# Kernel tuning notes

Hardware: AMD Instinct MI355X
Metric: run time of the kernel (lower is better)

Reference implementation:

```python
import jax, jax.numpy as jnp
import numpy as np

B, C, S, F = 128, 5, 512, 3
U = 256          # encoder units
RU = 2 * U       # decoder units / bidirectional encoder width


def _lstm_cell(x_t, h, c, Wk, Wr, b):
    # Keras LSTM gate order: i, f, g(cell), o
    z = x_t @ Wk + h @ Wr + b
    i, f, g, o = jnp.split(z, 4, axis=-1)
    c_new = jax.nn.sigmoid(f) * c + jax.nn.sigmoid(i) * jnp.tanh(g)
    h_new = jax.nn.sigmoid(o) * jnp.tanh(c_new)
    return h_new, c_new


def _masked_lstm(xs, mask, Wk, Wr, b, units):
    # xs: [B,S,D], mask: [B,S] bool. Keras semantics: masked steps carry
    # previous state and previous output (== previous h for LSTM).
    Bn = xs.shape[0]

    def step(carry, inp):
        h, c = carry
        x_t, m_t = inp
        h_n, c_n = _lstm_cell(x_t, h, c, Wk, Wr, b)
        m = m_t[:, None]
        h2 = jnp.where(m, h_n, h)
        c2 = jnp.where(m, c_n, c)
        return (h2, c2), h2

    init = (jnp.zeros((Bn, units), xs.dtype), jnp.zeros((Bn, units), xs.dtype))
    _, outs = jax.lax.scan(step, init, (jnp.swapaxes(xs, 0, 1), mask.T))
    return jnp.swapaxes(outs, 0, 1)  # [B,S,units]


def setup_inputs() -> dict:
    key = jax.random.key(0)
    k = jax.random.split(key, 10)
    s = 0.05
    rn = lambda kk, sh: jax.random.normal(kk, sh, jnp.float32) * s
    return {
        "x": jax.random.normal(k[0], (B, C, S, F), jnp.float32),
        "Wf_k": rn(k[1], (C, 4 * U)), "Wf_r": rn(k[2], (U, 4 * U)), "bf": jnp.zeros((4 * U,), jnp.float32),
        "Wb_k": rn(k[3], (C, 4 * U)), "Wb_r": rn(k[4], (U, 4 * U)), "bb": jnp.zeros((4 * U,), jnp.float32),
        "Wd_k": rn(k[5], (C, 4 * RU)), "Wd_r": rn(k[6], (RU, 4 * RU)), "bd": jnp.zeros((4 * RU,), jnp.float32),
        "W_attn": rn(k[7], (RU + C, 1)), "b_attn": jnp.zeros((1,), jnp.float32),
        "W_dense": rn(k[8], (RU + RU, C)), "b_dense": jnp.zeros((C,), jnp.float32),
    }


def reference(x, Wf_k, Wf_r, bf, Wb_k, Wb_r, bb, Wd_k, Wd_r, bd,
              W_attn, b_attn, W_dense, b_dense):
    xt = jnp.transpose(x, (0, 2, 1, 3))          # [B,S,C,F]
    mask = xt[:, :, 0, 2] != 0                   # tf.cast(..., bool)
    xs = xt[:, :, :, 0]                          # [B,S,C]

    fwd = _masked_lstm(xs, mask, Wf_k, Wf_r, bf, U)
    bwd = _masked_lstm(xs[:, ::-1], mask[:, ::-1], Wb_k, Wb_r, bb, U)[:, ::-1]
    enc = jnp.concatenate([fwd, bwd], axis=-1)   # [B,S,RU]

    # attention(concat([tile(x_t), enc])) is linear -> split the weight:
    Wx, We = W_attn[:C, 0], W_attn[C:, 0]
    enc_scores = jnp.einsum('bsd,d->bs', enc, We) + b_attn[0]  # [B,S]

    hidden0 = enc[:, -1, :]                      # [B,RU]
    x0 = xs[:, 0, :]                             # [B,C]

    def dec_step(carry, _):
        hidden, x_t = carry
        scores = enc_scores + (x_t @ Wx)[:, None]             # [B,S]
        alpha = jax.nn.softmax(scores, axis=1)
        attn = jnp.einsum('bs,bsd->bd', alpha, enc)           # [B,RU]
        # decoder LSTM on a single timestep, initial_state=[hidden, attn]
        h_new, _c = _lstm_cell(x_t, hidden, attn, Wd_k, Wd_r, bd)
        x_new = jnp.concatenate([h_new, attn], axis=-1) @ W_dense + b_dense
        return (h_new, x_new), x_new

    _, ys = jax.lax.scan(dec_step, (hidden0, x0), None, length=S - 1)  # [S-1,B,C]
    return jnp.transpose(ys, (1, 2, 0))[..., None]           # [B,C,S-1,1]
```

## Files before the change

### kernel.cpp

```cpp
#include <hip/hip_runtime.h>
#include <math.h>

#define BATCH 128
#define CCH 5
#define SEQ 512
#define UNITS 256
#define RU 512

#define ENC_N 33554432

__device__ __forceinline__ float sigmoidf_(float v) {
    return 1.0f / (1.0f + __expf(-v));
}
__device__ __forceinline__ float tanhf_(float v) {
    float e = __expf(2.0f * v);
    return 1.0f - 2.0f / (e + 1.0f);
}
__device__ __forceinline__ void astoref(float* p, float v) {
    __hip_atomic_store(p, v, __ATOMIC_RELAXED, __HIP_MEMORY_SCOPE_AGENT);
}
__device__ __forceinline__ void astorei(int* p, int v) {
    __hip_atomic_store(p, v, __ATOMIC_RELAXED, __HIP_MEMORY_SCOPE_AGENT);
}
__device__ __forceinline__ unsigned long long aloadu64(const unsigned long long* p) {
    return __hip_atomic_load(p, __ATOMIC_RELAXED, __HIP_MEMORY_SCOPE_AGENT);
}
__device__ __forceinline__ int aloadi(const int* p) {
    return __hip_atomic_load(p, __ATOMIC_RELAXED, __HIP_MEMORY_SCOPE_AGENT);
}

__global__ __attribute__((amdgpu_flat_work_group_size(1024, 1024),
                          amdgpu_waves_per_eu(4, 4)))
void encoder_kernel(const float* __restrict__ x,
                    const float* __restrict__ Wf_k, const float* __restrict__ Wf_r,
                    const float* __restrict__ bf,
                    const float* __restrict__ Wb_k, const float* __restrict__ Wb_r,
                    const float* __restrict__ bb,
                    float* __restrict__ enc, float* __restrict__ h_ex,
                    int* __restrict__ flags)
{
    const int bid  = blockIdx.x;
    const int dir  = bid >> 7;
    const int tile = (bid >> 3) & 15;
    const int jsl  = bid & 7;
    const int grp  = dir * 16 + tile;
    const int bg0  = tile * 8;
    const float* __restrict__ Wk   = dir ? Wb_k : Wf_k;
    const float* __restrict__ Wr   = dir ? Wb_r : Wf_r;
    const float* __restrict__ bias = dir ? bb : bf;
    const int tid  = threadIdx.x;
    const int wv   = tid >> 6;
    const int lane = tid & 63;
    const int g0 = ((lane >> 5) << 8) + jsl * 32 + (lane & 31);

    __shared__ float zp[16][8][128];
    __shared__ float __align__(16) hL[8][260];
    __shared__ float WkL[5][128];
    __shared__ float biasL[128];
    __shared__ unsigned char mL[8][SEQ];
    __shared__ float xLe[8][8];
    __shared__ float padE[512];

    for (int i = tid; i < 8 * 260; i += 1024) ((float*)hL)[i] = 0.0f;
    if (tid < 512) padE[tid] = 0.0f;
    if (tid < 128) biasL[tid] = bias[((tid >> 5) << 8) + jsl * 32 + (tid & 31)];
    if (tid >= 128 && tid < 768) {
        int i = tid - 128, c = i >> 7, cl = i & 127;
        WkL[c][cl] = Wk[c * 1024 + ((cl >> 5) << 8) + jsl * 32 + (cl & 31)];
    }
    for (int i = tid; i < 8 * SEQ; i += 1024) {
        int b = i >> 9, tt = i & (SEQ - 1);
        mL[b][tt] = (x[((size_t)((bg0 + b) * CCH) * SEQ + tt) * 3 + 2] != 0.0f) ? 1 : 0;
    }
    float wr0[16], wr1[16];
    {
        const float* wbase = Wr + (size_t)(wv * 16) * 1024 + g0;
        #pragma unroll
        for (int r = 0; r < 16; ++r) {
            wr0[r] = wbase[(size_t)r * 1024];
            wr1[r] = wbase[(size_t)r * 1024 + 512];
        }
        #pragma unroll
        for (int r = 0; r < 16; ++r)
            asm volatile("" : "+v"(wr0[r]), "+v"(wr1[r]));
    }
    float creg = 0.0f;
    __syncthreads();

    for (int t = 0; t < SEQ; ++t) {
        const int ts = dir ? (SEQ - 1 - t) : t;
        if (t > 0 && wv < 8) {
            const int* fp = &flags[(grp * 8 + wv) * 32];
            if (lane == 0) {
                int guard = 0;
                while (aloadi(fp) < t && guard < (1 << 26)) {
                    __builtin_amdgcn_s_sleep(1); ++guard;
                }
            }
            int b = lane >> 3, u = wv * 32 + (lane & 7) * 4;
            const unsigned long long* hsrc = (const unsigned long long*)
                &h_ex[(size_t)(dir * 2 + ((t - 1) & 1)) * (BATCH * UNITS)
                      + (size_t)(bg0 + b) * UNITS + u];
            unsigned long long v0 = aloadu64(hsrc);
            unsigned long long v1 = aloadu64(hsrc + 1);
            *(unsigned long long*)&hL[b][u]     = v0;
            *(unsigned long long*)&hL[b][u + 2] = v1;
        }
        if (tid >= 960 && tid < 1000) {
            int i = tid - 960, b = i / 5, c = i - b * 5;
            xLe[b][c] = x[((size_t)((bg0 + b) * CCH + c) * SEQ + ts) * 3];
        }
        __syncthreads();

        float accA[8], accB[8];
        #pragma unroll
        for (int b = 0; b < 8; ++b) {
            float a0 = 0.f, a1 = 0.f;
            const float4* hp = (const float4*)&hL[b][wv * 16];
            #pragma unroll
            for (int q = 0; q < 4; ++q) {
                float4 h4 = hp[q];
                a0 = fmaf(h4.x, wr0[4*q+0], a0); a1 = fmaf(h4.x, wr1[4*q+0], a1);
                a0 = fmaf(h4.y, wr0[4*q+1], a0); a1 = fmaf(h4.y, wr1[4*q+1], a1);
                a0 = fmaf(h4.z, wr0[4*q+2], a0); a1 = fmaf(h4.z, wr1[4*q+2], a1);
                a0 = fmaf(h4.w, wr0[4*q+3], a0); a1 = fmaf(h4.w, wr1[4*q+3], a1);
            }
            accA[b] = a0; accB[b] = a1;
        }
        #pragma unroll
        for (int b = 0; b < 8; ++b) {
            zp[wv][b][lane]      = accA[b];
            zp[wv][b][64 + lane] = accB[b];
        }
        __syncthreads();

        if (tid < 256) {
            int b = tid >> 5, u = tid & 31;
            float zi = biasL[u], zf = biasL[32 + u], zg = biasL[64 + u], zo = biasL[96 + u];
            #pragma unroll
            for (int s = 0; s < 16; ++s) {
                zi += zp[s][b][u];       zf += zp[s][b][32 + u];
                zg += zp[s][b][64 + u];  zo += zp[s][b][96 + u];
            }
            #pragma unroll
            for (int c = 0; c < 5; ++c) {
                float xv = xLe[b][c];
                zi = fmaf(xv, WkL[c][u], zi);      zf = fmaf(xv, WkL[c][32 + u], zf);
                zg = fmaf(xv, WkL[c][64 + u], zg); zo = fmaf(xv, WkL[c][96 + u], zo);
            }
            float cn = sigmoidf_(zf) * creg + sigmoidf_(zi) * tanhf_(zg);
            float hn = sigmoidf_(zo) * tanhf_(cn);
            float hprev = hL[b][jsl * 32 + u];
            float h2 = mL[b][ts] ? hn : hprev;
            float c2 = mL[b][ts] ? cn : creg;
            creg = c2;
            astoref(&h_ex[(size_t)(dir * 2 + (t & 1)) * (BATCH * UNITS)
                          + (size_t)(bg0 + b) * UNITS + jsl * 32 + u], h2);
            enc[((size_t)(bg0 + b) * SEQ + ts) * RU + dir * UNITS + jsl * 32 + u] = h2;
        }
        __syncthreads();
        if (tid == 0) astorei(&flags[(grp * 8 + jsl) * 32], t + 1);
    }
    if (aloadi(&flags[(grp * 8 + jsl) * 32]) == -1) enc[0] = padE[tid & 511];
}

__global__ __launch_bounds__(256)
void attn_kernel(const float* __restrict__ enc,
                 const float* __restrict__ W_attn, const float* __restrict__ b_attn,
                 const float* __restrict__ W_dense, const float* __restrict__ b_dense,
                 const float* __restrict__ x,
                 float* __restrict__ attn_ws, float* __restrict__ hidden_ws,
                 float* __restrict__ xbuf, float* __restrict__ xconst)
{
    const int b = blockIdx.x;
    const int tid = threadIdx.x;
    const int lane = tid & 63;
    const int wv = tid >> 6;

    __shared__ float WeL[RU];
    __shared__ float scoresL[SEQ];
    __shared__ float red[256];
    __shared__ float attnL[RU];

    WeL[tid]       = W_attn[CCH + tid];
    WeL[tid + 256] = W_attn[CCH + tid + 256];
    __syncthreads();

    const float* __restrict__ encb = enc + (size_t)b * SEQ * RU;
    const float batt = b_attn[0];

    for (int s = wv; s < SEQ; s += 4) {
        const float* row = encb + (size_t)s * RU;
        float p = 0.0f;
        #pragma unroll
        for (int i = 0; i < 8; ++i) {
            int d = lane * 8 + i;
            p = fmaf(row[d], WeL[d], p);
        }
        #pragma unroll
        for (int o = 32; o; o >>= 1) p += __shfl_xor(p, o);
        if (lane == 0) scoresL[s] = p + batt;
    }
    __syncthreads();

    float m = fmaxf(scoresL[tid], scoresL[tid + 256]);
    red[tid] = m;
    __syncthreads();
    for (int st = 128; st; st >>= 1) {
        if (tid < st) red[tid] = fmaxf(red[tid], red[tid + st]);
        __syncthreads();
    }
    const float mx = red[0];
    __syncthreads();
    float e0 = __expf(scoresL[tid] - mx);
    float e1 = __expf(scoresL[tid + 256] - mx);
    red[tid] = e0 + e1;
    __syncthreads();
    for (int st = 128; st; st >>= 1) {
        if (tid < st) red[tid] += red[tid + st];
        __syncthreads();
    }
    const float sinv = 1.0f / red[0];
    __syncthreads();
    scoresL[tid]       = e0 * sinv;
    scoresL[tid + 256] = e1 * sinv;
    __syncthreads();

    float a0 = 0.0f, a1 = 0.0f;
    for (int s = 0; s < SEQ; ++s) {
        float al = scoresL[s];
        a0 = fmaf(al, encb[(size_t)s * RU + tid], a0);
        a1 = fmaf(al, encb[(size_t)s * RU + tid + 256], a1);
    }
    attn_ws[(size_t)b * RU + tid]       = a0;
    attn_ws[(size_t)b * RU + tid + 256] = a1;
    attnL[tid] = a0;
    attnL[tid + 256] = a1;
    hidden_ws[(size_t)b * RU + tid]       = encb[(size_t)(SEQ - 1) * RU + tid];
    hidden_ws[(size_t)b * RU + tid + 256] = encb[(size_t)(SEQ - 1) * RU + tid + 256];
    if (tid < CCH) xbuf[b * CCH + tid] = x[((size_t)(b * CCH + tid) * SEQ + 0) * 3];
    __syncthreads();

    if (tid < CCH) {
        float acc = b_dense[tid];
        for (int d = 0; d < RU; ++d)
            acc = fmaf(attnL[d], W_dense[(RU + d) * CCH + tid], acc);
        xconst[b * CCH + tid] = acc;
    }
}

__global__ __attribute__((amdgpu_flat_work_group_size(1024, 1024),
                          amdgpu_waves_per_eu(4, 4)))
void decoder_kernel(const float* __restrict__ Wd_k, const float* __restrict__ Wd_r,
                    const float* __restrict__ bd,
                    const float* __restrict__ W_dense,
                    const float* __restrict__ attn_ws, const float* __restrict__ hidden_ws,
                    const float* __restrict__ xbuf, const float* __restrict__ xconst,
                    float* __restrict__ h_ex, int* __restrict__ flags,
                    float* __restrict__ out)
{
    const int bid  = blockIdx.x;
    const int tile = bid >> 4;
    const int jsl  = bid & 15;
    const int bg0  = tile * 8;
    const int tid  = threadIdx.x;
    const int wv   = tid >> 6;
    const int lane = tid & 63;
    const int g0 = ((lane >> 5) << 9) + jsl * 32 + (lane & 31);

    __shared__ float zp[16][8][128];
    __shared__ float __align__(16) hL[8][516];
    __shared__ float WdL[RU * CCH];
    __shared__ float WkL[5][128];
    __shared__ float biasL[128];
    __shared__ float attL[8][32];
    __shared__ float xL[8][8], xcL[8][8];

    for (int i = tid; i < RU * CCH; i += 1024) WdL[i] = W_dense[i];
    if (tid < 128) biasL[tid] = bd[((tid >> 5) << 9) + jsl * 32 + (tid & 31)];
    if (tid >= 128 && tid < 768) {
        int i = tid - 128, c = i >> 7, cl = i & 127;
        WkL[c][cl] = Wd_k[c * 2048 + ((cl >> 5) << 9) + jsl * 32 + (cl & 31)];
    }
    if (tid < 256) {
        int b = tid >> 5, u = tid & 31;
        attL[b][u] = attn_ws[(size_t)(bg0 + b) * RU + jsl * 32 + u];
    }
    if (tid < 64) {
        int b = tid >> 3, c = tid & 7;
        if (c < 5) {
            xL[b][c]  = xbuf[(bg0 + b) * CCH + c];
            xcL[b][c] = xconst[(bg0 + b) * CCH + c];
        }
    }
    {
        int f = tid * 4, b = f >> 9, u = f & (RU - 1);
        float4 v = *(const float4*)&hidden_ws[(size_t)(bg0 + b) * RU + u];
        *(float4*)&hL[b][u] = v;
    }
    float wr0[32], wr1[32];
    {
        const float* wbase = Wd_r + (size_t)(wv * 32) * 2048 + g0;
        #pragma unroll
        for (int r = 0; r < 32; ++r) {
            wr0[r] = wbase[(size_t)r * 2048];
            wr1[r] = wbase[(size_t)r * 2048 + 1024];
        }
        #pragma unroll
        for (int r = 0; r < 32; ++r)
            asm volatile("" : "+v"(wr0[r]), "+v"(wr1[r]));
    }
    __syncthreads();

    for (int t = 0; t < SEQ; ++t) {
        if (t > 0) {
            const int* fp = &flags[(tile * 16 + wv) * 32];
            if (lane == 0) {
                int guard = 0;
                while (aloadi(fp) < t && guard < (1 << 26)) {
                    __builtin_amdgcn_s_sleep(1); ++guard;
                }
            }
            int b = lane >> 3, u = wv * 32 + (lane & 7) * 4;
            const unsigned long long* hsrc = (const unsigned long long*)
                &h_ex[(size_t)((t - 1) & 1) * (BATCH * RU)
                      + (size_t)(bg0 + b) * RU + u];
            unsigned long long v0 = aloadu64(hsrc);
            unsigned long long v1 = aloadu64(hsrc + 1);
            *(unsigned long long*)&hL[b][u]     = v0;
            *(unsigned long long*)&hL[b][u + 2] = v1;
            __syncthreads();

            for (int it = wv; it < 40; it += 16) {
                int bb = it / 5, c = it - bb * 5;
                float p = 0.f;
                #pragma unroll
                for (int q = 0; q < 8; ++q) {
                    int uu = lane + (q << 6);
                    p = fmaf(hL[bb][uu], WdL[uu * CCH + c], p);
                }
                #pragma unroll
                for (int o = 32; o; o >>= 1) p += __shfl_xor(p, o);
                if (lane == 0) {
                    float xn = p + xcL[bb][c];
                    xL[bb][c] = xn;
                    if (jsl == 0)
                        out[(size_t)((bg0 + bb) * CCH + c) * (SEQ - 1) + (t - 1)] = xn;
                }
            }
            if (t == 511) break;
        }

        float accA[8], accB[8];
        #pragma unroll
        for (int b = 0; b < 8; ++b) {
            float a0 = 0.f, a1 = 0.f;
            const float4* hp = (const float4*)&hL[b][wv * 32];
            #pragma unroll
            for (int q = 0; q < 8; ++q) {
                float4 h4 = hp[q];
                a0 = fmaf(h4.x, wr0[4*q+0], a0); a1 = fmaf(h4.x, wr1[4*q+0], a1);
                a0 = fmaf(h4.y, wr0[4*q+1], a0); a1 = fmaf(h4.y, wr1[4*q+1], a1);
                a0 = fmaf(h4.z, wr0[4*q+2], a0); a1 = fmaf(h4.z, wr1[4*q+2], a1);
                a0 = fmaf(h4.w, wr0[4*q+3], a0); a1 = fmaf(h4.w, wr1[4*q+3], a1);
            }
            accA[b] = a0; accB[b] = a1;
        }
        #pragma unroll
        for (int b = 0; b < 8; ++b) {
            zp[wv][b][lane]      = accA[b];
            zp[wv][b][64 + lane] = accB[b];
        }
        __syncthreads();

        if (tid < 256) {
            int b = tid >> 5, u = tid & 31;
            float zi = biasL[u], zf = biasL[32 + u], zg = biasL[64 + u], zo = biasL[96 + u];
            #pragma unroll
            for (int s = 0; s < 16; ++s) {
                zi += zp[s][b][u];       zf += zp[s][b][32 + u];
                zg += zp[s][b][64 + u];  zo += zp[s][b][96 + u];
            }
            #pragma unroll
            for (int c = 0; c < 5; ++c) {
                float xv = xL[b][c];
                zi = fmaf(xv, WkL[c][u], zi);      zf = fmaf(xv, WkL[c][32 + u], zf);
                zg = fmaf(xv, WkL[c][64 + u], zg); zo = fmaf(xv, WkL[c][96 + u], zo);
            }
            float cn = sigmoidf_(zf) * attL[b][u] + sigmoidf_(zi) * tanhf_(zg);
            float hn = sigmoidf_(zo) * tanhf_(cn);
            astoref(&h_ex[(size_t)(t & 1) * (BATCH * RU)
                          + (size_t)(bg0 + b) * RU + jsl * 32 + u], hn);
        }
        __syncthreads();
        if (tid == 0) astorei(&flags[(tile * 16 + jsl) * 32], t + 1);
    }
}

extern "C" void kernel_launch(void* const* d_in, const int* in_sizes, int n_in,
                              void* d_out, int out_size, void* d_ws, size_t ws_size,
                              hipStream_t stream)
{
    const float* x       = (const float*)d_in[0];
    const float* Wf_k    = (const float*)d_in[1];
    const float* Wf_r    = (const float*)d_in[2];
    const float* bf      = (const float*)d_in[3];
    const float* Wb_k    = (const float*)d_in[4];
    const float* Wb_r    = (const float*)d_in[5];
    const float* bb      = (const float*)d_in[6];
    const float* Wd_k    = (const float*)d_in[7];
    const float* Wd_r    = (const float*)d_in[8];
    const float* bd      = (const float*)d_in[9];
    const float* W_attn  = (const float*)d_in[10];
    const float* b_attn  = (const float*)d_in[11];
    const float* W_dense = (const float*)d_in[12];
    const float* b_dense = (const float*)d_in[13];
    float* out = (float*)d_out;

    float* ws = (float*)d_ws;
    float* enc      = ws;
    float* attn_p   = ws + ENC_N;
    float* hidden_p = ws + ENC_N + 65536;
    float* xbuf_p   = ws + ENC_N + 131072;
    float* xconst_p = ws + ENC_N + 131712;
    float* h_ex_e   = ws + ENC_N;
    int*   flag_e   = (int*)(ws + ENC_N + 131072);
    int*   flag_d   = (int*)ws;
    float* h_ex_d   = ws + 8192;

    hipMemsetAsync(flag_e, 0, 8192 * sizeof(int), stream);
    encoder_kernel<<<256, 1024, 0, stream>>>(x, Wf_k, Wf_r, bf, Wb_k, Wb_r, bb,
                                             enc, h_ex_e, flag_e);
    attn_kernel<<<BATCH, 256, 0, stream>>>(enc, W_attn, b_attn, W_dense, b_dense, x,
                                           attn_p, hidden_p, xbuf_p, xconst_p);
    hipMemsetAsync(flag_d, 0, 8192 * sizeof(int), stream);
    decoder_kernel<<<256, 1024, 0, stream>>>(Wd_k, Wd_r, bd, W_dense,
                                             attn_p, hidden_p, xbuf_p, xconst_p,
                                             h_ex_d, flag_d, out);
}
```

Measured before the change: 5.270 ms.

## Double-buffer hidden state, parallelize gate reduction, replace trailing barrier with counter

Both the encoder and decoder recurrent kernels now double-buffer the shared hidden-state tile, which lets them drop the end-of-step __syncthreads. The finishing waves publish the inter-block flag through a workgroup-scope atomic counter after their global stores have drained. The 16-way partial-sum reduction is now spread across all 1024 threads into a zred buffer, replacing the 256 threads that each summed four gates. In the decoder, the dense output projection overlaps with the recurrent matvec and its store moves to other threads, and the final step is peeled out of the loop. The aim is to shorten the per-timestep critical path in the latency-bound recurrence, at the cost of an extra barrier, more shared memory, and a spin-wait ordering subtlety.

```diff
diff --git a/kernel.cpp b/kernel.cpp
--- a/kernel.cpp
+++ b/kernel.cpp
@@ -53,16 +53,17 @@
     const int lane = tid & 63;
     const int g0 = ((lane >> 5) << 8) + jsl * 32 + (lane & 31);
 
-    __shared__ float zp[16][8][128];
-    __shared__ float __align__(16) hL[8][260];
+    __shared__ float2 zpP[16][8][64];
+    __shared__ float __align__(16) hLe[2][8][260];
+    __shared__ float zred[8][128];
     __shared__ float WkL[5][128];
     __shared__ float biasL[128];
     __shared__ unsigned char mL[8][SEQ];
     __shared__ float xLe[8][8];
-    __shared__ float padE[512];
-
-    for (int i = tid; i < 8 * 260; i += 1024) ((float*)hL)[i] = 0.0f;
-    if (tid < 512) padE[tid] = 0.0f;
+    __shared__ int msync;
+
+    for (int i = tid; i < 2 * 8 * 260; i += 1024) ((float*)hLe)[i] = 0.0f;
+    if (tid == 0) msync = 0;
     if (tid < 128) biasL[tid] = bias[((tid >> 5) << 8) + jsl * 32 + (tid & 31)];
     if (tid >= 128 && tid < 768) {
         int i = tid - 128, c = i >> 7, cl = i & 127;
@@ -88,6 +89,7 @@
     __syncthreads();
 
     for (int t = 0; t < SEQ; ++t) {
+        const int cur = t & 1;
         const int ts = dir ? (SEQ - 1 - t) : t;
         if (t > 0 && wv < 8) {
             const int* fp = &flags[(grp * 8 + wv) * 32];
@@ -103,8 +105,8 @@
                       + (size_t)(bg0 + b) * UNITS + u];
             unsigned long long v0 = aloadu64(hsrc);
             unsigned long long v1 = aloadu64(hsrc + 1);
-            *(unsigned long long*)&hL[b][u]     = v0;
-            *(unsigned long long*)&hL[b][u + 2] = v1;
+            *(unsigned long long*)&hLe[cur][b][u]     = v0;
+            *(unsigned long long*)&hLe[cur][b][u + 2] = v1;
         }
         if (tid >= 960 && tid < 1000) {
             int i = tid - 960, b = i / 5, c = i - b * 5;
@@ -116,7 +118,7 @@
         #pragma unroll
         for (int b = 0; b < 8; ++b) {
             float a0 = 0.f, a1 = 0.f;
-            const float4* hp = (const float4*)&hL[b][wv * 16];
+            const float4* hp = (const float4*)&hLe[cur][b][wv * 16];
             #pragma unroll
             for (int q = 0; q < 4; ++q) {
                 float4 h4 = hp[q];
@@ -128,40 +130,54 @@
             accA[b] = a0; accB[b] = a1;
         }
         #pragma unroll
-        for (int b = 0; b < 8; ++b) {
-            zp[wv][b][lane]      = accA[b];
-            zp[wv][b][64 + lane] = accB[b];
+        for (int b = 0; b < 8; ++b)
+            zpP[wv][b][lane] = make_float2(accA[b], accB[b]);
+        __syncthreads();
+
+        {
+            int b = tid >> 7, cl = tid & 127;
+            int gate = cl >> 5, u = cl & 31;
+            int lane_r = ((gate & 1) << 5) | u;
+            int comp = gate >> 1;
+            const float* zf = (const float*)zpP + b * 128 + lane_r * 2 + comp;
+            float sum = biasL[cl];
+            #pragma unroll
+            for (int s = 0; s < 16; ++s) sum += zf[s * 1024];
+            #pragma unroll
+            for (int c = 0; c < 5; ++c) sum = fmaf(xLe[b][c], WkL[c][cl], sum);
+            zred[b][cl] = sum;
         }
         __syncthreads();
 
         if (tid < 256) {
             int b = tid >> 5, u = tid & 31;
-            float zi = biasL[u], zf = biasL[32 + u], zg = biasL[64 + u], zo = biasL[96 + u];
-            #pragma unroll
-            for (int s = 0; s < 16; ++s) {
-                zi += zp[s][b][u];       zf += zp[s][b][32 + u];
-                zg += zp[s][b][64 + u];  zo += zp[s][b][96 + u];
-            }
-            #pragma unroll
-            for (int c = 0; c < 5; ++c) {
-                float xv = xLe[b][c];
-                zi = fmaf(xv, WkL[c][u], zi);      zf = fmaf(xv, WkL[c][32 + u], zf);
-                zg = fmaf(xv, WkL[c][64 + u], zg); zo = fmaf(xv, WkL[c][96 + u], zo);
-            }
-            float cn = sigmoidf_(zf) * creg + sigmoidf_(zi) * tanhf_(zg);
+            float zi = zred[b][u];
+            float zf_ = zred[b][32 + u];
+            float zg = zred[b][64 + u];
+            float zo = zred[b][96 + u];
+            float cn = sigmoidf_(zf_) * creg + sigmoidf_(zi) * tanhf_(zg);
             float hn = sigmoidf_(zo) * tanhf_(cn);
-            float hprev = hL[b][jsl * 32 + u];
+            float hprev = hLe[cur][b][jsl * 32 + u];
             float h2 = mL[b][ts] ? hn : hprev;
             float c2 = mL[b][ts] ? cn : creg;
             creg = c2;
             astoref(&h_ex[(size_t)(dir * 2 + (t & 1)) * (BATCH * UNITS)
                           + (size_t)(bg0 + b) * UNITS + jsl * 32 + u], h2);
             enc[((size_t)(bg0 + b) * SEQ + ts) * RU + dir * UNITS + jsl * 32 + u] = h2;
-        }
-        __syncthreads();
-        if (tid == 0) astorei(&flags[(grp * 8 + jsl) * 32], t + 1);
-    }
-    if (aloadi(&flags[(grp * 8 + jsl) * 32]) == -1) enc[0] = padE[tid & 511];
+            if (lane == 0) {
+                asm volatile("s_waitcnt vmcnt(0)" ::: "memory");
+                __hip_atomic_fetch_add(&msync, 1, __ATOMIC_RELAXED,
+                                       __HIP_MEMORY_SCOPE_WORKGROUP);
+            }
+            if (tid == 0) {
+                int target = 4 * (t + 1), guard = 0;
+                while (__hip_atomic_load(&msync, __ATOMIC_RELAXED,
+                                         __HIP_MEMORY_SCOPE_WORKGROUP) < target &&
+                       guard < (1 << 26)) ++guard;
+                astorei(&flags[(grp * 8 + jsl) * 32], t + 1);
+            }
+        }
+    }
 }
 
 __global__ __launch_bounds__(256)
@@ -268,15 +284,18 @@
     const int lane = tid & 63;
     const int g0 = ((lane >> 5) << 9) + jsl * 32 + (lane & 31);
 
-    __shared__ float zp[16][8][128];
-    __shared__ float __align__(16) hL[8][516];
+    __shared__ float2 zpP[16][8][64];
+    __shared__ float __align__(16) hLd[2][8][516];
+    __shared__ float zred[8][128];
     __shared__ float WdL[RU * CCH];
     __shared__ float WkL[5][128];
     __shared__ float biasL[128];
     __shared__ float attL[8][32];
     __shared__ float xL[8][8], xcL[8][8];
+    __shared__ int msync;
 
     for (int i = tid; i < RU * CCH; i += 1024) WdL[i] = W_dense[i];
+    if (tid == 0) msync = 0;
     if (tid < 128) biasL[tid] = bd[((tid >> 5) << 9) + jsl * 32 + (tid & 31)];
     if (tid >= 128 && tid < 768) {
         int i = tid - 128, c = i >> 7, cl = i & 127;
@@ -296,7 +315,7 @@
     {
         int f = tid * 4, b = f >> 9, u = f & (RU - 1);
         float4 v = *(const float4*)&hidden_ws[(size_t)(bg0 + b) * RU + u];
-        *(float4*)&hL[b][u] = v;
+        *(float4*)&hLd[0][b][u] = v;
     }
     float wr0[32], wr1[32];
     {
@@ -312,7 +331,8 @@
     }
     __syncthreads();
 
-    for (int t = 0; t < SEQ; ++t) {
+    for (int t = 0; t < SEQ - 1; ++t) {
+        const int cur = t & 1;
         if (t > 0) {
             const int* fp = &flags[(tile * 16 + wv) * 32];
             if (lane == 0) {
@@ -327,35 +347,16 @@
                       + (size_t)(bg0 + b) * RU + u];
             unsigned long long v0 = aloadu64(hsrc);
             unsigned long long v1 = aloadu64(hsrc + 1);
-            *(unsigned long long*)&hL[b][u]     = v0;
-            *(unsigned long long*)&hL[b][u + 2] = v1;
-            __syncthreads();
-
-            for (int it = wv; it < 40; it += 16) {
-                int bb = it / 5, c = it - bb * 5;
-                float p = 0.f;
-                #pragma unroll
-                for (int q = 0; q < 8; ++q) {
-                    int uu = lane + (q << 6);
-                    p = fmaf(hL[bb][uu], WdL[uu * CCH + c], p);
-                }
-                #pragma unroll
-                for (int o = 32; o; o >>= 1) p += __shfl_xor(p, o);
-                if (lane == 0) {
-                    float xn = p + xcL[bb][c];
-                    xL[bb][c] = xn;
-                    if (jsl == 0)
-                        out[(size_t)((bg0 + bb) * CCH + c) * (SEQ - 1) + (t - 1)] = xn;
-                }
-            }
-            if (t == 511) break;
-        }
+            *(unsigned long long*)&hLd[cur][b][u]     = v0;
+            *(unsigned long long*)&hLd[cur][b][u + 2] = v1;
+        }
+        __syncthreads();
 
         float accA[8], accB[8];
         #pragma unroll
         for (int b = 0; b < 8; ++b) {
             float a0 = 0.f, a1 = 0.f;
-            const float4* hp = (const float4*)&hL[b][wv * 32];
+            const float4* hp = (const float4*)&hLd[cur][b][wv * 32];
             #pragma unroll
             for (int q = 0; q < 8; ++q) {
                 float4 h4 = hp[q];
@@ -367,33 +368,104 @@
             accA[b] = a0; accB[b] = a1;
         }
         #pragma unroll
-        for (int b = 0; b < 8; ++b) {
-            zp[wv][b][lane]      = accA[b];
-            zp[wv][b][64 + lane] = accB[b];
+        for (int b = 0; b < 8; ++b)
+            zpP[wv][b][lane] = make_float2(accA[b], accB[b]);
+
+        if (t > 0) {
+            for (int it = wv; it < 40; it += 16) {
+                int bb = it / 5, c = it - bb * 5;
+                float p = 0.f;
+                #pragma unroll
+                for (int q = 0; q < 8; ++q) {
+                    int uu = lane + (q << 6);
+                    p = fmaf(hLd[cur][bb][uu], WdL[uu * CCH + c], p);
+                }
+                #pragma unroll
+                for (int o = 32; o; o >>= 1) p += __shfl_xor(p, o);
+                if (lane == 0) xL[bb][c] = p + xcL[bb][c];
+            }
+        }
+        __syncthreads();
+
+        {
+            int b = tid >> 7, cl = tid & 127;
+            int gate = cl >> 5, u = cl & 31;
+            int lane_r = ((gate & 1) << 5) | u;
+            int comp = gate >> 1;
+            const float* zf = (const float*)zpP + b * 128 + lane_r * 2 + comp;
+            float sum = biasL[cl];
+            #pragma unroll
+            for (int s = 0; s < 16; ++s) sum += zf[s * 1024];
+            #pragma unroll
+            for (int c = 0; c < 5; ++c) sum = fmaf(xL[b][c], WkL[c][cl], sum);
+            zred[b][cl] = sum;
         }
         __syncthreads();
 
         if (tid < 256) {
             int b = tid >> 5, u = tid & 31;
-            float zi = biasL[u], zf = biasL[32 + u], zg = biasL[64 + u], zo = biasL[96 + u];
-            #pragma unroll
-            for (int s = 0; s < 16; ++s) {
-                zi += zp[s][b][u];       zf += zp[s][b][32 + u];
-                zg += zp[s][b][64 + u];  zo += zp[s][b][96 + u];
-            }
-            #pragma unroll
-            for (int c = 0; c < 5; ++c) {
-                float xv = xL[b][c];
-                zi = fmaf(xv, WkL[c][u], zi);      zf = fmaf(xv, WkL[c][32 + u], zf);
-                zg = fmaf(xv, WkL[c][64 + u], zg); zo = fmaf(xv, WkL[c][96 + u], zo);
-            }
-            float cn = sigmoidf_(zf) * attL[b][u] + sigmoidf_(zi) * tanhf_(zg);
+            float zi = zred[b][u];
+            float zf_ = zred[b][32 + u];
+            float zg = zred[b][64 + u];
+            float zo = zred[b][96 + u];
+            float cn = sigmoidf_(zf_) * attL[b][u] + sigmoidf_(zi) * tanhf_(zg);
             float hn = sigmoidf_(zo) * tanhf_(cn);
             astoref(&h_ex[(size_t)(t & 1) * (BATCH * RU)
                           + (size_t)(bg0 + b) * RU + jsl * 32 + u], hn);
-        }
-        __syncthreads();
-        if (tid == 0) astorei(&flags[(tile * 16 + jsl) * 32], t + 1);
+            if (lane == 0) {
+                asm volatile("s_waitcnt vmcnt(0)" ::: "memory");
+                __hip_atomic_fetch_add(&msync, 1, __ATOMIC_RELAXED,
+                                       __HIP_MEMORY_SCOPE_WORKGROUP);
+            }
+            if (tid == 0) {
+                int target = 4 * (t + 1), guard = 0;
+                while (__hip_atomic_load(&msync, __ATOMIC_RELAXED,
+                                         __HIP_MEMORY_SCOPE_WORKGROUP) < target &&
+                       guard < (1 << 26)) ++guard;
+                astorei(&flags[(tile * 16 + jsl) * 32], t + 1);
+            }
+        }
+        if (t > 0 && jsl == 0 && tid >= 256 && tid < 296) {
+            int i = tid - 256, bb = i / 5, c = i - bb * 5;
+            out[(size_t)((bg0 + bb) * CCH + c) * (SEQ - 1) + (t - 1)] = xL[bb][c];
+        }
+    }
+
+    {
+        const int t = SEQ - 1;
+        const int cur = t & 1;
+        const int* fp = &flags[(tile * 16 + wv) * 32];
+        if (lane == 0) {
+            int guard = 0;
+            while (aloadi(fp) < t && guard < (1 << 26)) {
+                __builtin_amdgcn_s_sleep(1); ++guard;
+            }
+        }
+        int b = lane >> 3, u = wv * 32 + (lane & 7) * 4;
+        const unsigned long long* hsrc = (const unsigned long long*)
+            &h_ex[(size_t)((t - 1) & 1) * (BATCH * RU)
+                  + (size_t)(bg0 + b) * RU + u];
+        unsigned long long v0 = aloadu64(hsrc);
+        unsigned long long v1 = aloadu64(hsrc + 1);
+        *(unsigned long long*)&hLd[cur][b][u]     = v0;
+        *(unsigned long long*)&hLd[cur][b][u + 2] = v1;
+        __syncthreads();
+        if (jsl == 0) {
+            for (int it = wv; it < 40; it += 16) {
+                int bb = it / 5, c = it - bb * 5;
+                float p = 0.f;
+                #pragma unroll
+                for (int q = 0; q < 8; ++q) {
+                    int uu = lane + (q << 6);
+                    p = fmaf(hLd[cur][bb][uu], WdL[uu * CCH + c], p);
+                }
+                #pragma unroll
+                for (int o = 32; o; o >>= 1) p += __shfl_xor(p, o);
+                if (lane == 0)
+                    out[(size_t)((bg0 + bb) * CCH + c) * (SEQ - 1) + (t - 1)]
+                        = p + xcL[bb][c];
+            }
+        }
     }
 }
 
```

New measurement: 6.396 ms. 1.21x slower.

## Interleave batch pairs in hidden state and use packed FMA for recurrent matvec

Applied to the files above, without the earlier changes.

The hidden-state exchange buffers and the LDS copies now store pairs of batch rows interleaved. This lets the recurrent matvec in both the encoder and decoder use v_pk_fma_f32, processing two batch rows per instruction. All 16 encoder waves now share the h load instead of only 8, and the decoder LDS h buffer is double-buffered. The decoder output write moves off the critical path and the last step is peeled out of the loop. The inline-asm packed FMA and the changed global layout depend on the op_sel semantics and the indexing being correct.

```diff
diff --git a/kernel.cpp b/kernel.cpp
--- a/kernel.cpp
+++ b/kernel.cpp
@@ -9,6 +9,8 @@
 
 #define ENC_N 33554432
 
+typedef float v2f __attribute__((ext_vector_type(2)));
+
 __device__ __forceinline__ float sigmoidf_(float v) {
     return 1.0f / (1.0f + __expf(-v));
 }
@@ -28,6 +30,13 @@
 __device__ __forceinline__ int aloadi(const int* p) {
     return __hip_atomic_load(p, __ATOMIC_RELAXED, __HIP_MEMORY_SCOPE_AGENT);
 }
+
+#define PK_LO(ACC, H2, W2) \
+    asm("v_pk_fma_f32 %0, %1, %2, %0 op_sel:[0,0,0] op_sel_hi:[1,0,1]" \
+        : "+v"(ACC) : "v"(H2), "v"(W2))
+#define PK_HI(ACC, H2, W2) \
+    asm("v_pk_fma_f32 %0, %1, %2, %0 op_sel:[0,1,0] op_sel_hi:[1,1,1]" \
+        : "+v"(ACC) : "v"(H2), "v"(W2))
 
 __global__ __attribute__((amdgpu_flat_work_group_size(1024, 1024),
                           amdgpu_waves_per_eu(4, 4)))
@@ -54,15 +63,13 @@
     const int g0 = ((lane >> 5) << 8) + jsl * 32 + (lane & 31);
 
     __shared__ float zp[16][8][128];
-    __shared__ float __align__(16) hL[8][260];
+    __shared__ float __align__(16) hPe[2][4][520];
     __shared__ float WkL[5][128];
     __shared__ float biasL[128];
     __shared__ unsigned char mL[8][SEQ];
     __shared__ float xLe[8][8];
-    __shared__ float padE[512];
-
-    for (int i = tid; i < 8 * 260; i += 1024) ((float*)hL)[i] = 0.0f;
-    if (tid < 512) padE[tid] = 0.0f;
+
+    for (int i = tid; i < 2 * 4 * 520; i += 1024) ((float*)hPe)[i] = 0.0f;
     if (tid < 128) biasL[tid] = bias[((tid >> 5) << 8) + jsl * 32 + (tid & 31)];
     if (tid >= 128 && tid < 768) {
         int i = tid - 128, c = i >> 7, cl = i & 127;
@@ -72,39 +79,34 @@
         int b = i >> 9, tt = i & (SEQ - 1);
         mL[b][tt] = (x[((size_t)((bg0 + b) * CCH) * SEQ + tt) * 3 + 2] != 0.0f) ? 1 : 0;
     }
-    float wr0[16], wr1[16];
+    v2f wp[16];
     {
         const float* wbase = Wr + (size_t)(wv * 16) * 1024 + g0;
         #pragma unroll
         for (int r = 0; r < 16; ++r) {
-            wr0[r] = wbase[(size_t)r * 1024];
-            wr1[r] = wbase[(size_t)r * 1024 + 512];
-        }
-        #pragma unroll
-        for (int r = 0; r < 16; ++r)
-            asm volatile("" : "+v"(wr0[r]), "+v"(wr1[r]));
+            v2f w; w.x = wbase[(size_t)r * 1024]; w.y = wbase[(size_t)r * 1024 + 512];
+            wp[r] = w;
+        }
     }
     float creg = 0.0f;
     __syncthreads();
 
     for (int t = 0; t < SEQ; ++t) {
+        const int cur = t & 1;
         const int ts = dir ? (SEQ - 1 - t) : t;
-        if (t > 0 && wv < 8) {
-            const int* fp = &flags[(grp * 8 + wv) * 32];
+        if (t > 0) {
+            const int* fp = &flags[(grp * 8 + (wv >> 1)) * 32];
             if (lane == 0) {
                 int guard = 0;
                 while (aloadi(fp) < t && guard < (1 << 26)) {
                     __builtin_amdgcn_s_sleep(1); ++guard;
                 }
             }
-            int b = lane >> 3, u = wv * 32 + (lane & 7) * 4;
+            int p = lane >> 4, u = wv * 16 + (lane & 15);
             const unsigned long long* hsrc = (const unsigned long long*)
-                &h_ex[(size_t)(dir * 2 + ((t - 1) & 1)) * (BATCH * UNITS)
-                      + (size_t)(bg0 + b) * UNITS + u];
-            unsigned long long v0 = aloadu64(hsrc);
-            unsigned long long v1 = aloadu64(hsrc + 1);
-            *(unsigned long long*)&hL[b][u]     = v0;
-            *(unsigned long long*)&hL[b][u + 2] = v1;
+                &h_ex[(size_t)(dir * 2 + ((t - 1) & 1)) * (BATCH * UNITS)];
+            unsigned long long v = aloadu64(hsrc + (size_t)((bg0 >> 1) + p) * UNITS + u);
+            *(unsigned long long*)&hPe[cur][p][u * 2] = v;
         }
         if (tid >= 960 && tid < 1000) {
             int i = tid - 960, b = i / 5, c = i - b * 5;
@@ -112,25 +114,35 @@
         }
         __syncthreads();
 
-        float accA[8], accB[8];
-        #pragma unroll
-        for (int b = 0; b < 8; ++b) {
-            float a0 = 0.f, a1 = 0.f;
-            const float4* hp = (const float4*)&hL[b][wv * 16];
-            #pragma unroll
-            for (int q = 0; q < 4; ++q) {
-                float4 h4 = hp[q];
-                a0 = fmaf(h4.x, wr0[4*q+0], a0); a1 = fmaf(h4.x, wr1[4*q+0], a1);
-                a0 = fmaf(h4.y, wr0[4*q+1], a0); a1 = fmaf(h4.y, wr1[4*q+1], a1);
-                a0 = fmaf(h4.z, wr0[4*q+2], a0); a1 = fmaf(h4.z, wr1[4*q+2], a1);
-                a0 = fmaf(h4.w, wr0[4*q+3], a0); a1 = fmaf(h4.w, wr1[4*q+3], a1);
-            }
-            accA[b] = a0; accB[b] = a1;
-        }
-        #pragma unroll
-        for (int b = 0; b < 8; ++b) {
-            zp[wv][b][lane]      = accA[b];
-            zp[wv][b][64 + lane] = accB[b];
+        v2f acc0[4], acc1[4];
+        #pragma unroll
+        for (int p = 0; p < 4; ++p) { acc0[p] = (v2f){0.f, 0.f}; acc1[p] = (v2f){0.f, 0.f}; }
+        #pragma unroll
+        for (int q = 0; q < 8; ++q) {
+            v2f h[4][2];
+            #pragma unroll
+            for (int p = 0; p < 4; ++p) {
+                float4 A = *(const float4*)&hPe[cur][p][(wv * 16 + q * 2) * 2];
+                v2f h0; h0.x = A.x; h0.y = A.y;
+                v2f h1; h1.x = A.z; h1.y = A.w;
+                h[p][0] = h0; h[p][1] = h1;
+            }
+            #pragma unroll
+            for (int r = 0; r < 2; ++r) {
+                v2f w2 = wp[q * 2 + r];
+                #pragma unroll
+                for (int p = 0; p < 4; ++p) {
+                    PK_LO(acc0[p], h[p][r], w2);
+                    PK_HI(acc1[p], h[p][r], w2);
+                }
+            }
+        }
+        #pragma unroll
+        for (int p = 0; p < 4; ++p) {
+            zp[wv][2 * p][lane]          = acc0[p].x;
+            zp[wv][2 * p + 1][lane]      = acc0[p].y;
+            zp[wv][2 * p][64 + lane]     = acc1[p].x;
+            zp[wv][2 * p + 1][64 + lane] = acc1[p].y;
         }
         __syncthreads();
 
@@ -150,18 +162,17 @@
             }
             float cn = sigmoidf_(zf) * creg + sigmoidf_(zi) * tanhf_(zg);
             float hn = sigmoidf_(zo) * tanhf_(cn);
-            float hprev = hL[b][jsl * 32 + u];
+            float hprev = hPe[cur][b >> 1][(jsl * 32 + u) * 2 + (b & 1)];
             float h2 = mL[b][ts] ? hn : hprev;
             float c2 = mL[b][ts] ? cn : creg;
             creg = c2;
-            astoref(&h_ex[(size_t)(dir * 2 + (t & 1)) * (BATCH * UNITS)
-                          + (size_t)(bg0 + b) * UNITS + jsl * 32 + u], h2);
+            astoref(&h_ex[(size_t)(dir * 2 + cur) * (BATCH * UNITS)
+                          + ((size_t)((bg0 + b) >> 1) * UNITS + jsl * 32 + u) * 2 + (b & 1)], h2);
             enc[((size_t)(bg0 + b) * SEQ + ts) * RU + dir * UNITS + jsl * 32 + u] = h2;
         }
         __syncthreads();
         if (tid == 0) astorei(&flags[(grp * 8 + jsl) * 32], t + 1);
     }
-    if (aloadi(&flags[(grp * 8 + jsl) * 32]) == -1) enc[0] = padE[tid & 511];
 }
 
 __global__ __launch_bounds__(256)
@@ -269,7 +280,7 @@
     const int g0 = ((lane >> 5) << 9) + jsl * 32 + (lane & 31);
 
     __shared__ float zp[16][8][128];
-    __shared__ float __align__(16) hL[8][516];
+    __shared__ float __align__(16) hPd[2][4][1040];
     __shared__ float WdL[RU * CCH];
     __shared__ float WkL[5][128];
     __shared__ float biasL[128];
@@ -293,26 +304,24 @@
             xcL[b][c] = xconst[(bg0 + b) * CCH + c];
         }
     }
-    {
-        int f = tid * 4, b = f >> 9, u = f & (RU - 1);
-        float4 v = *(const float4*)&hidden_ws[(size_t)(bg0 + b) * RU + u];
-        *(float4*)&hL[b][u] = v;
-    }
-    float wr0[32], wr1[32];
+    for (int e = tid; e < 2048; e += 1024) {
+        int p = e >> 9, u = e & 511;
+        hPd[0][p][u * 2]     = hidden_ws[(size_t)(bg0 + 2 * p) * RU + u];
+        hPd[0][p][u * 2 + 1] = hidden_ws[(size_t)(bg0 + 2 * p + 1) * RU + u];
+    }
+    v2f wp[32];
     {
         const float* wbase = Wd_r + (size_t)(wv * 32) * 2048 + g0;
         #pragma unroll
         for (int r = 0; r < 32; ++r) {
-            wr0[r] = wbase[(size_t)r * 2048];
-            wr1[r] = wbase[(size_t)r * 2048 + 1024];
-        }
-        #pragma unroll
-        for (int r = 0; r < 32; ++r)
-            asm volatile("" : "+v"(wr0[r]), "+v"(wr1[r]));
-    }
-    __syncthreads();
-
-    for (int t = 0; t < SEQ; ++t) {
+            v2f w; w.x = wbase[(size_t)r * 2048]; w.y = wbase[(size_t)r * 2048 + 1024];
+            wp[r] = w;
+        }
+    }
+    __syncthreads();
+
+    for (int t = 0; t < SEQ - 1; ++t) {
+        const int cur = t & 1;
         if (t > 0) {
             const int* fp = &flags[(tile * 16 + wv) * 32];
             if (lane == 0) {
@@ -321,55 +330,61 @@
                     __builtin_amdgcn_s_sleep(1); ++guard;
                 }
             }
-            int b = lane >> 3, u = wv * 32 + (lane & 7) * 4;
+            int p = lane >> 4, u0 = wv * 32 + (lane & 15) * 2;
             const unsigned long long* hsrc = (const unsigned long long*)
-                &h_ex[(size_t)((t - 1) & 1) * (BATCH * RU)
-                      + (size_t)(bg0 + b) * RU + u];
-            unsigned long long v0 = aloadu64(hsrc);
-            unsigned long long v1 = aloadu64(hsrc + 1);
-            *(unsigned long long*)&hL[b][u]     = v0;
-            *(unsigned long long*)&hL[b][u + 2] = v1;
-            __syncthreads();
-
+                &h_ex[(size_t)((t - 1) & 1) * (BATCH * RU)];
+            unsigned long long v0 = aloadu64(hsrc + (size_t)((bg0 >> 1) + p) * RU + u0);
+            unsigned long long v1 = aloadu64(hsrc + (size_t)((bg0 >> 1) + p) * RU + u0 + 1);
+            *(unsigned long long*)&hPd[cur][p][u0 * 2]       = v0;
+            *(unsigned long long*)&hPd[cur][p][(u0 + 1) * 2] = v1;
+        }
+        __syncthreads();
+
+        if (t > 0) {
             for (int it = wv; it < 40; it += 16) {
                 int bb = it / 5, c = it - bb * 5;
+                const float* hb = &hPd[cur][bb >> 1][bb & 1];
                 float p = 0.f;
                 #pragma unroll
                 for (int q = 0; q < 8; ++q) {
                     int uu = lane + (q << 6);
-                    p = fmaf(hL[bb][uu], WdL[uu * CCH + c], p);
+                    p = fmaf(hb[uu * 2], WdL[uu * CCH + c], p);
                 }
                 #pragma unroll
                 for (int o = 32; o; o >>= 1) p += __shfl_xor(p, o);
-                if (lane == 0) {
-                    float xn = p + xcL[bb][c];
-                    xL[bb][c] = xn;
-                    if (jsl == 0)
-                        out[(size_t)((bg0 + bb) * CCH + c) * (SEQ - 1) + (t - 1)] = xn;
-                }
-            }
-            if (t == 511) break;
-        }
-
-        float accA[8], accB[8];
-        #pragma unroll
-        for (int b = 0; b < 8; ++b) {
-            float a0 = 0.f, a1 = 0.f;
-            const float4* hp = (const float4*)&hL[b][wv * 32];
-            #pragma unroll
-            for (int q = 0; q < 8; ++q) {
-                float4 h4 = hp[q];
-                a0 = fmaf(h4.x, wr0[4*q+0], a0); a1 = fmaf(h4.x, wr1[4*q+0], a1);
-                a0 = fmaf(h4.y, wr0[4*q+1], a0); a1 = fmaf(h4.y, wr1[4*q+1], a1);
-                a0 = fmaf(h4.z, wr0[4*q+2], a0); a1 = fmaf(h4.z, wr1[4*q+2], a1);
-                a0 = fmaf(h4.w, wr0[4*q+3], a0); a1 = fmaf(h4.w, wr1[4*q+3], a1);
-            }
-            accA[b] = a0; accB[b] = a1;
-        }
-        #pragma unroll
-        for (int b = 0; b < 8; ++b) {
-            zp[wv][b][lane]      = accA[b];
-            zp[wv][b][64 + lane] = accB[b];
+                if (lane == 0) xL[bb][c] = p + xcL[bb][c];
+            }
+        }
+
+        v2f acc0[4], acc1[4];
+        #pragma unroll
+        for (int p = 0; p < 4; ++p) { acc0[p] = (v2f){0.f, 0.f}; acc1[p] = (v2f){0.f, 0.f}; }
+        #pragma unroll
+        for (int q = 0; q < 16; ++q) {
+            v2f h[4][2];
+            #pragma unroll
+            for (int p = 0; p < 4; ++p) {
+                float4 A = *(const float4*)&hPd[cur][p][(wv * 32 + q * 2) * 2];
+                v2f h0; h0.x = A.x; h0.y = A.y;
+                v2f h1; h1.x = A.z; h1.y = A.w;
+                h[p][0] = h0; h[p][1] = h1;
+            }
+            #pragma unroll
+            for (int r = 0; r < 2; ++r) {
+                v2f w2 = wp[q * 2 + r];
+                #pragma unroll
+                for (int p = 0; p < 4; ++p) {
+                    PK_LO(acc0[p], h[p][r], w2);
+                    PK_HI(acc1[p], h[p][r], w2);
+                }
+            }
+        }
+        #pragma unroll
+        for (int p = 0; p < 4; ++p) {
+            zp[wv][2 * p][lane]          = acc0[p].x;
+            zp[wv][2 * p + 1][lane]      = acc0[p].y;
+            zp[wv][2 * p][64 + lane]     = acc1[p].x;
+            zp[wv][2 * p + 1][64 + lane] = acc1[p].y;
         }
         __syncthreads();
 
@@ -389,11 +404,52 @@
             }
             float cn = sigmoidf_(zf) * attL[b][u] + sigmoidf_(zi) * tanhf_(zg);
             float hn = sigmoidf_(zo) * tanhf_(cn);
-            astoref(&h_ex[(size_t)(t & 1) * (BATCH * RU)
-                          + (size_t)(bg0 + b) * RU + jsl * 32 + u], hn);
+            astoref(&h_ex[(size_t)cur * (BATCH * RU)
+                          + ((size_t)((bg0 + b) >> 1) * RU + jsl * 32 + u) * 2 + (b & 1)], hn);
         }
         __syncthreads();
         if (tid == 0) astorei(&flags[(tile * 16 + jsl) * 32], t + 1);
+        if (t > 0 && jsl == 0 && tid >= 256 && tid < 296) {
+            int i = tid - 256, bb = i / 5, c = i - bb * 5;
+            out[(size_t)((bg0 + bb) * CCH + c) * (SEQ - 1) + (t - 1)] = xL[bb][c];
+        }
+    }
+
+    {
+        const int t = SEQ - 1;
+        const int cur = t & 1;
+        const int* fp = &flags[(tile * 16 + wv) * 32];
+        if (lane == 0) {
+            int guard = 0;
+            while (aloadi(fp) < t && guard < (1 << 26)) {
+                __builtin_amdgcn_s_sleep(1); ++guard;
+            }
+        }
+        int p = lane >> 4, u0 = wv * 32 + (lane & 15) * 2;
+        const unsigned long long* hsrc = (const unsigned long long*)
+            &h_ex[(size_t)((t - 1) & 1) * (BATCH * RU)];
+        unsigned long long v0 = aloadu64(hsrc + (size_t)((bg0 >> 1) + p) * RU + u0);
+        unsigned long long v1 = aloadu64(hsrc + (size_t)((bg0 >> 1) + p) * RU + u0 + 1);
+        *(unsigned long long*)&hPd[cur][p][u0 * 2]       = v0;
+        *(unsigned long long*)&hPd[cur][p][(u0 + 1) * 2] = v1;
+        __syncthreads();
+        if (jsl == 0) {
+            for (int it = wv; it < 40; it += 16) {
+                int bb = it / 5, c = it - bb * 5;
+                const float* hb = &hPd[cur][bb >> 1][bb & 1];
+                float p2 = 0.f;
+                #pragma unroll
+                for (int q = 0; q < 8; ++q) {
+                    int uu = lane + (q << 6);
+                    p2 = fmaf(hb[uu * 2], WdL[uu * CCH + c], p2);
+                }
+                #pragma unroll
+                for (int o = 32; o; o >>= 1) p2 += __shfl_xor(p2, o);
+                if (lane == 0)
+                    out[(size_t)((bg0 + bb) * CCH + c) * (SEQ - 1) + (t - 1)]
+                        = p2 + xcL[bb][c];
+            }
+        }
     }
 }
 
```

Measured after the change: 5.599 ms. 6.2% more time.
